# Optimization experiments

Hardware: AMD Instinct MI355X
Metric: run time of the kernel (lower is better)

## Reference

```python
import jax, jax.numpy as jnp
import numpy as np

PRE, POST, BATCH, HIST = 1024, 1024, 256, 50
CONN_PROB = 0.1

def setup_inputs() -> dict:
    key = jax.random.key(0)
    k1, k2, k3, k4, k5 = jax.random.split(key, 5)
    pre_spikes = (jax.random.uniform(k1, (BATCH, PRE)) < 0.2).astype(jnp.float32)   # sparse spike trains
    post_spikes = (jax.random.uniform(k2, (BATCH, POST)) < 0.2).astype(jnp.float32)
    connectivity_mask = (jax.random.uniform(k3, (PRE, POST)) < CONN_PROB).astype(jnp.float32)
    synaptic_weights = jax.random.normal(k4, (PRE, POST), dtype=jnp.float32) * 0.1 * connectivity_mask
    correlation_history = jax.random.normal(k5, (PRE, POST, HIST), dtype=jnp.float32) * 0.01
    return {
        "pre_spikes": pre_spikes,
        "post_spikes": post_spikes,
        "synaptic_weights": synaptic_weights,
        "connectivity_mask": connectivity_mask,
        "correlation_history": correlation_history,
        "pre_activity": jnp.zeros((PRE,), jnp.float32),
        "post_activity": jnp.zeros((POST,), jnp.float32),
        "corr_index": 7,
    }

def reference(pre_spikes, post_spikes, synaptic_weights, connectivity_mask,
              correlation_history, pre_activity, post_activity, corr_index):
    # EMA of population activity (buffer updates in the torch module)
    pre_mean = pre_spikes.mean(axis=0)    # [pre]
    post_mean = post_spikes.mean(axis=0)  # [post]
    new_pre_activity = 0.99 * pre_activity + 0.01 * pre_mean
    new_post_activity = 0.99 * post_activity + 0.01 * post_mean

    # circular-buffer scatter: write current outer-product correlation at slot idx
    idx = corr_index % correlation_history.shape[-1]
    current_correlation = jnp.outer(pre_mean, post_mean)            # [pre, post]
    new_history = correlation_history.at[:, :, idx].set(current_correlation)

    # masked matmul: fuse elementwise mask into the GEMM operand
    effective_weights = synaptic_weights * connectivity_mask        # [pre, post]
    synaptic_current = pre_spikes @ effective_weights               # [batch, post]

    # connectivity_info['average_correlation'] (plasticity disabled: current_time <= 1.0)
    average_correlation = new_history.mean(axis=-1)                 # [pre, post]

    return (synaptic_current, new_pre_activity, new_post_activity,
            average_correlation, new_history)
```

## Files before the change

### kernel.cpp

```cpp
#include <hip/hip_runtime.h>

#define PRE   1024
#define POST  1024
#define BATCH 256
#define HIST  50
#define NPAIR (PRE * POST)

typedef float nf4 __attribute__((ext_vector_type(4)));

#define MCOLS 16
__global__ __launch_bounds__(256) void means_kernel(
    const float* __restrict__ pre_spikes,
    const float* __restrict__ post_spikes,
    const float* __restrict__ pre_activity,
    const float* __restrict__ post_activity,
    float* __restrict__ ws_means,
    float* __restrict__ out_pre_act,
    float* __restrict__ out_post_act)
{
    __shared__ float red[256];
    int tid = threadIdx.x;
    int blk = blockIdx.x;
    bool is_pre = blk < 64;
    const float* mat = is_pre ? pre_spikes : post_spikes;
    const float* act = is_pre ? pre_activity : post_activity;
    float* out_act   = is_pre ? out_pre_act : out_post_act;
    float* ws        = is_pre ? ws_means : ws_means + PRE;
    int col0 = (blk & 63) * MCOLS;

    int col = col0 + (tid & 15);
    int chunk = tid >> 4;
    float s = 0.f;
#pragma unroll
    for (int r = chunk * 16; r < chunk * 16 + 16; ++r)
        s += mat[r * 1024 + col];
    red[tid] = s;
    __syncthreads();
    if (tid < 16) {
        float t = 0.f;
#pragma unroll
        for (int k = 0; k < 16; ++k)
            t += red[k * 16 + tid];
        float m = t * (1.0f / BATCH);
        int c = col0 + tid;
        ws[c] = m;
        out_act[c] = 0.99f * act[c] + 0.01f * m;
    }
}

#define GBM 64
#define GBN 64
#define GBK 16
#define GKSPLIT 8
#define GLD 68
__global__ __launch_bounds__(256) void gemm_kernel(
    const float* __restrict__ A,
    const float* __restrict__ W,
    const float* __restrict__ Mk,
    float* __restrict__ C,
    float* __restrict__ Cpart,
    int use_part)
{
    __shared__ __align__(16) float As[GBK * GLD];
    __shared__ __align__(16) float Bs[GBK * GLD];
    int tid = threadIdx.x;
    int bn = blockIdx.x;
    int bm = blockIdx.y;
    int bz = blockIdx.z;
    int kbase = bz * (PRE / GKSPLIT);

    int ar = tid >> 2;
    int ak = (tid & 3) << 2;
    int bk = tid >> 4;
    int bn4 = (tid & 15) << 2;
    int tn4 = (tid & 15) << 2;
    int tm4 = (tid >> 4) << 2;

    const float* Ap = &A[(bm * GBM + ar) * PRE + kbase + ak];
    const float* Wp = &W [(size_t)(kbase + bk) * POST + bn * GBN + bn4];
    const float* Mp = &Mk[(size_t)(kbase + bk) * POST + bn * GBN + bn4];

    float acc[4][4] = {};

    for (int k0 = 0; k0 < PRE / GKSPLIT; k0 += GBK) {
        float4 av = *(const float4*)(Ap + k0);
        float4 wv = *(const float4*)(Wp + (size_t)k0 * POST);
        float4 mv = *(const float4*)(Mp + (size_t)k0 * POST);
        wv.x *= mv.x; wv.y *= mv.y; wv.z *= mv.z; wv.w *= mv.w;
        __syncthreads();
        As[(ak + 0) * GLD + ar] = av.x;
        As[(ak + 1) * GLD + ar] = av.y;
        As[(ak + 2) * GLD + ar] = av.z;
        As[(ak + 3) * GLD + ar] = av.w;
        *(float4*)&Bs[bk * GLD + bn4] = wv;
        __syncthreads();
#pragma unroll
        for (int kk = 0; kk < GBK; ++kk) {
            float4 a4 = *(const float4*)&As[kk * GLD + tm4];
            float4 b4 = *(const float4*)&Bs[kk * GLD + tn4];
            const float* ap = (const float*)&a4;
            const float* bp = (const float*)&b4;
#pragma unroll
            for (int i = 0; i < 4; ++i)
#pragma unroll
                for (int j = 0; j < 4; ++j)
                    acc[i][j] += ap[i] * bp[j];
        }
    }
    if (use_part) {
        float* dst = &Cpart[(size_t)bz * (BATCH * POST)
                            + (size_t)(bm * GBM + tm4) * POST + bn * GBN + tn4];
#pragma unroll
        for (int i = 0; i < 4; ++i) {
            float4 r; r.x = acc[i][0]; r.y = acc[i][1]; r.z = acc[i][2]; r.w = acc[i][3];
            *(float4*)(dst + (size_t)i * POST) = r;
        }
    } else {
#pragma unroll
        for (int i = 0; i < 4; ++i)
#pragma unroll
            for (int j = 0; j < 4; ++j)
                atomicAdd(&C[(size_t)(bm * GBM + tm4 + i) * POST + bn * GBN + tn4 + j],
                          acc[i][j]);
    }
}

__global__ __launch_bounds__(256) void gemm_reduce_kernel(
    const float* __restrict__ Cpart,
    float* __restrict__ C)
{
    int g = blockIdx.x * 256 + threadIdx.x;
    const nf4* p4 = (const nf4*)Cpart;
    nf4 s = p4[g];
#pragma unroll
    for (int z = 1; z < GKSPLIT; ++z)
        s += p4[(size_t)z * (BATCH * POST / 4) + g];
    ((nf4*)C)[g] = s;
}

#define PPB 128
#define HTHREADS 320
#define NIT 5
__global__ __launch_bounds__(HTHREADS) void history_kernel(
    const float* __restrict__ hist_in,
    const int*   __restrict__ corr_index,
    const float* __restrict__ ws_means,
    float* __restrict__ hist_out,
    float* __restrict__ avg_out)
{
    __shared__ __align__(16) float tile[PPB * HIST + 2];
    int tid = threadIdx.x;
    int p0 = blockIdx.x * PPB;
    int idx = ((corr_index[0] % HIST) + HIST) % HIST;

    const nf4* in4   = (const nf4*)(hist_in + (size_t)p0 * HIST);
    nf4*       out4  = (nf4*)(hist_out + (size_t)p0 * HIST);
    nf4*       tile4 = (nf4*)tile;

    nf4 v[NIT];
#pragma unroll
    for (int it = 0; it < NIT; ++it)
        v[it] = __builtin_nontemporal_load(&in4[it * HTHREADS + tid]);

#pragma unroll
    for (int it = 0; it < NIT; ++it) {
        int fl = it * HTHREADS + tid;
        int r0 = 4 * fl;
        int pl = r0 / HIST;
        int t0 = r0 - pl * HIST;
        int d  = idx - t0;
        int d2 = idx + HIST - t0;
        bool needA = ((unsigned)d) < 4u;
        bool needB = (d2 < 4);
        float corr = 0.f;
        if (needA | needB) {
            int pair = needA ? (p0 + pl) : (p0 + pl + 1);
            corr = ws_means[pair >> 10] * ws_means[PRE + (pair & (POST - 1))];
        }
        nf4 w = v[it];
        w.x = (d == 0) ? corr : w.x;
        w.y = (d == 1) ? corr : w.y;
        w.z = (d == 2 || d2 == 2) ? corr : w.z;
        w.w = (d == 3 || d2 == 3) ? corr : w.w;
        v[it] = w;
        tile4[fl] = w;
    }
    __syncthreads();

#pragma unroll
    for (int it = 0; it < NIT; ++it)
        __builtin_nontemporal_store(v[it], &out4[it * HTHREADS + tid]);

    if (tid < 2 * PPB) {
        int pl   = tid >> 1;
        int half = tid & 1;
        const float2* tp = (const float2*)&tile[pl * HIST];
        float s = 0.f;
#pragma unroll
        for (int k = 0; k < 13; ++k) {
            int f2 = 2 * k + half;
            float2 w = tp[f2];
            if (f2 < 25) s += w.x + w.y;
        }
        s += __shfl_xor(s, 1);
        if (half == 0)
            __builtin_nontemporal_store(s * (1.0f / HIST), &avg_out[p0 + pl]);
    }
}

extern "C" void kernel_launch(void* const* d_in, const int* in_sizes, int n_in,
                              void* d_out, int out_size, void* d_ws, size_t ws_size,
                              hipStream_t stream)
{
    const float* pre_spikes  = (const float*)d_in[0];
    const float* post_spikes = (const float*)d_in[1];
    const float* W           = (const float*)d_in[2];
    const float* Mk          = (const float*)d_in[3];
    const float* hist        = (const float*)d_in[4];
    const float* pre_act     = (const float*)d_in[5];
    const float* post_act    = (const float*)d_in[6];
    const int*   corr_index  = (const int*)d_in[7];

    float* out = (float*)d_out;
    float* out_current  = out;
    float* out_pre_act  = out + 262144;
    float* out_post_act = out + 263168;
    float* out_avg      = out + 264192;
    float* out_hist     = out + 1312768;

    float* ws_means = (float*)d_ws;
    float* cpart    = ws_means + 4096;
    size_t ws_need  = (size_t)4096 * 4 + (size_t)GKSPLIT * BATCH * POST * 4;
    int use_part    = ws_size >= ws_need;

    means_kernel<<<128, 256, 0, stream>>>(
        pre_spikes, post_spikes, pre_act, post_act,
        ws_means, out_pre_act, out_post_act);

    if (!use_part)
        (void)hipMemsetAsync(out_current, 0, (size_t)BATCH * POST * sizeof(float), stream);

    gemm_kernel<<<dim3(POST / GBN, BATCH / GBM, GKSPLIT), 256, 0, stream>>>(
        pre_spikes, W, Mk, out_current, cpart, use_part);

    if (use_part)
        gemm_reduce_kernel<<<BATCH * POST / 4 / 256, 256, 0, stream>>>(cpart, out_current);

    history_kernel<<<NPAIR / PPB, HTHREADS, 0, stream>>>(
        hist, corr_index, ws_means, out_hist, out_avg);
}
```

Baseline: 373.4 us.

## Merge means+GEMM and reduce+history into two combined kernel launches

Folds the means kernel and split-K GEMM into one launch by partitioning blockIdx, and folds the split-K reduction into the history kernel as extra leading blocks. This cuts four launches to two, removing launch gaps and letting small independent work overlap with larger work. The reduce blocks now use 320 threads with a bounds check, and the combined kernels may need more registers or shared memory per block.

```diff
diff --git a/kernel.cpp b/kernel.cpp
--- a/kernel.cpp
+++ b/kernel.cpp
@@ -9,64 +9,65 @@
 typedef float nf4 __attribute__((ext_vector_type(4)));
 
 #define MCOLS 16
-__global__ __launch_bounds__(256) void means_kernel(
+#define GBM 64
+#define GBN 64
+#define GBK 16
+#define GKSPLIT 8
+#define GLD 68
+
+__global__ __launch_bounds__(256) void fusedA_kernel(
     const float* __restrict__ pre_spikes,
     const float* __restrict__ post_spikes,
     const float* __restrict__ pre_activity,
     const float* __restrict__ post_activity,
     float* __restrict__ ws_means,
     float* __restrict__ out_pre_act,
-    float* __restrict__ out_post_act)
-{
-    __shared__ float red[256];
-    int tid = threadIdx.x;
-    int blk = blockIdx.x;
-    bool is_pre = blk < 64;
-    const float* mat = is_pre ? pre_spikes : post_spikes;
-    const float* act = is_pre ? pre_activity : post_activity;
-    float* out_act   = is_pre ? out_pre_act : out_post_act;
-    float* ws        = is_pre ? ws_means : ws_means + PRE;
-    int col0 = (blk & 63) * MCOLS;
-
-    int col = col0 + (tid & 15);
-    int chunk = tid >> 4;
-    float s = 0.f;
-#pragma unroll
-    for (int r = chunk * 16; r < chunk * 16 + 16; ++r)
-        s += mat[r * 1024 + col];
-    red[tid] = s;
-    __syncthreads();
-    if (tid < 16) {
-        float t = 0.f;
-#pragma unroll
-        for (int k = 0; k < 16; ++k)
-            t += red[k * 16 + tid];
-        float m = t * (1.0f / BATCH);
-        int c = col0 + tid;
-        ws[c] = m;
-        out_act[c] = 0.99f * act[c] + 0.01f * m;
-    }
-}
-
-#define GBM 64
-#define GBN 64
-#define GBK 16
-#define GKSPLIT 8
-#define GLD 68
-__global__ __launch_bounds__(256) void gemm_kernel(
-    const float* __restrict__ A,
+    float* __restrict__ out_post_act,
     const float* __restrict__ W,
     const float* __restrict__ Mk,
     float* __restrict__ C,
     float* __restrict__ Cpart,
     int use_part)
 {
+    int tid = threadIdx.x;
+
+    if (blockIdx.x < 128) {
+        __shared__ float red[256];
+        int blk = blockIdx.x;
+        bool is_pre = blk < 64;
+        const float* mat = is_pre ? pre_spikes : post_spikes;
+        const float* act = is_pre ? pre_activity : post_activity;
+        float* out_act   = is_pre ? out_pre_act : out_post_act;
+        float* ws        = is_pre ? ws_means : ws_means + PRE;
+        int col0 = (blk & 63) * MCOLS;
+
+        int col = col0 + (tid & 15);
+        int chunk = tid >> 4;
+        float s = 0.f;
+#pragma unroll
+        for (int r = chunk * 16; r < chunk * 16 + 16; ++r)
+            s += mat[r * 1024 + col];
+        red[tid] = s;
+        __syncthreads();
+        if (tid < 16) {
+            float t = 0.f;
+#pragma unroll
+            for (int k = 0; k < 16; ++k)
+                t += red[k * 16 + tid];
+            float m = t * (1.0f / BATCH);
+            int c = col0 + tid;
+            ws[c] = m;
+            out_act[c] = 0.99f * act[c] + 0.01f * m;
+        }
+        return;
+    }
+
     __shared__ __align__(16) float As[GBK * GLD];
     __shared__ __align__(16) float Bs[GBK * GLD];
-    int tid = threadIdx.x;
-    int bn = blockIdx.x;
-    int bm = blockIdx.y;
-    int bz = blockIdx.z;
+    int id = blockIdx.x - 128;
+    int bn = id & 15;
+    int bm = (id >> 4) & 3;
+    int bz = id >> 6;
     int kbase = bz * (PRE / GKSPLIT);
 
     int ar = tid >> 2;
@@ -76,7 +77,7 @@
     int tn4 = (tid & 15) << 2;
     int tm4 = (tid >> 4) << 2;
 
-    const float* Ap = &A[(bm * GBM + ar) * PRE + kbase + ak];
+    const float* Ap = &pre_spikes[(bm * GBM + ar) * PRE + kbase + ak];
     const float* Wp = &W [(size_t)(kbase + bk) * POST + bn * GBN + bn4];
     const float* Mp = &Mk[(size_t)(kbase + bk) * POST + bn * GBN + bn4];
 
@@ -125,32 +126,38 @@
     }
 }
 
-__global__ __launch_bounds__(256) void gemm_reduce_kernel(
-    const float* __restrict__ Cpart,
-    float* __restrict__ C)
-{
-    int g = blockIdx.x * 256 + threadIdx.x;
-    const nf4* p4 = (const nf4*)Cpart;
-    nf4 s = p4[g];
-#pragma unroll
-    for (int z = 1; z < GKSPLIT; ++z)
-        s += p4[(size_t)z * (BATCH * POST / 4) + g];
-    ((nf4*)C)[g] = s;
-}
-
 #define PPB 128
 #define HTHREADS 320
 #define NIT 5
-__global__ __launch_bounds__(HTHREADS) void history_kernel(
+#define NRED 205
+
+__global__ __launch_bounds__(HTHREADS) void fusedB_kernel(
     const float* __restrict__ hist_in,
     const int*   __restrict__ corr_index,
     const float* __restrict__ ws_means,
     float* __restrict__ hist_out,
-    float* __restrict__ avg_out)
+    float* __restrict__ avg_out,
+    const float* __restrict__ Cpart,
+    float* __restrict__ C,
+    int nred)
 {
+    int tid = threadIdx.x;
+
+    if ((int)blockIdx.x < nred) {
+        int g = blockIdx.x * HTHREADS + tid;
+        if (g < BATCH * POST / 4) {
+            const nf4* p4 = (const nf4*)Cpart;
+            nf4 s = p4[g];
+#pragma unroll
+            for (int z = 1; z < GKSPLIT; ++z)
+                s += p4[(size_t)z * (BATCH * POST / 4) + g];
+            ((nf4*)C)[g] = s;
+        }
+        return;
+    }
+
     __shared__ __align__(16) float tile[PPB * HIST + 2];
-    int tid = threadIdx.x;
-    int p0 = blockIdx.x * PPB;
+    int p0 = (blockIdx.x - nred) * PPB;
     int idx = ((corr_index[0] % HIST) + HIST) % HIST;
 
     const nf4* in4   = (const nf4*)(hist_in + (size_t)p0 * HIST);
@@ -233,19 +240,16 @@
     size_t ws_need  = (size_t)4096 * 4 + (size_t)GKSPLIT * BATCH * POST * 4;
     int use_part    = ws_size >= ws_need;
 
-    means_kernel<<<128, 256, 0, stream>>>(
-        pre_spikes, post_spikes, pre_act, post_act,
-        ws_means, out_pre_act, out_post_act);
-
     if (!use_part)
         (void)hipMemsetAsync(out_current, 0, (size_t)BATCH * POST * sizeof(float), stream);
 
-    gemm_kernel<<<dim3(POST / GBN, BATCH / GBM, GKSPLIT), 256, 0, stream>>>(
-        pre_spikes, W, Mk, out_current, cpart, use_part);
-
-    if (use_part)
-        gemm_reduce_kernel<<<BATCH * POST / 4 / 256, 256, 0, stream>>>(cpart, out_current);
-
-    history_kernel<<<NPAIR / PPB, HTHREADS, 0, stream>>>(
-        hist, corr_index, ws_means, out_hist, out_avg);
+    fusedA_kernel<<<128 + 512, 256, 0, stream>>>(
+        pre_spikes, post_spikes, pre_act, post_act,
+        ws_means, out_pre_act, out_post_act,
+        W, Mk, out_current, cpart, use_part);
+
+    int nred = use_part ? NRED : 0;
+    fusedB_kernel<<<nred + NPAIR / PPB, HTHREADS, 0, stream>>>(
+        hist, corr_index, ws_means, out_hist, out_avg,
+        cpart, out_current, nred);
 }
```

Result: no change. 370.4 us (-0.8%).
